# Kernel tuning notes

Measured on AMD Instinct MI355X. Metric: run time of the kernel, lower is better.

## Reference

```python
import jax, jax.numpy as jnp
from jax import lax
import numpy as np

NUM_ITER = 20
H, W = 512, 512
EPS = 1e-8

# fixed (non-trainable) kernels from the module
_GX = (1.0 / 6.0) * jnp.array([[-1.0, 0.0, 1.0], [-2.0, 0.0, 2.0], [-1.0, 0.0, 1.0]], jnp.float32)
_GY = (1.0 / 6.0) * jnp.array([[-1.0, -2.0, -1.0], [0.0, 0.0, 0.0], [1.0, 2.0, 1.0]], jnp.float32)
_GXU = jnp.array([[0.0, 0.0, 0.0], [0.0, -1.0, 1.0], [0.0, 0.0, 0.0]], jnp.float32)
_GYU = jnp.array([[0.0, 0.0, 0.0], [0.0, -1.0, 0.0], [0.0, 1.0, 0.0]], jnp.float32)
K_GRAD = jnp.stack([_GX, _GY])[:, None]    # (2,1,3,3) image-gradient conv
K_GRADU = jnp.stack([_GXU, _GYU])[:, None]  # (2,1,3,3) flow-gradient conv
K_AVG = jnp.ones((1, 1, 3, 3), jnp.float32) / 9.0  # AvgPool2d(3,1,1), count_include_pad
P33 = ((1, 1), (1, 1))
P13 = ((0, 0), (1, 1))
P31 = ((1, 1), (0, 0))


def _conv(x, w, pad):
    return lax.conv_general_dilated(x, w, (1, 1), padding=pad,
                                    dimension_numbers=('NCHW', 'OIHW', 'NCHW'))


def setup_inputs() -> dict:
    key = jax.random.key(0)
    x = jax.random.uniform(key, (4, 2, H, W), dtype=jnp.float32)  # two frames per sample
    return {
        'x': x,
        'lam': jnp.array([0.15], jnp.float32),
        'tau': jnp.array([0.25], jnp.float32),
        'theta': jnp.array([0.3], jnp.float32),
        'wx': jnp.array([[-1.0, 1.0, 0.0]], jnp.float32),   # trainable div_x kernel
        'wy': jnp.array([[-1.0], [1.0], [0.0]], jnp.float32),  # trainable div_y kernel
    }


def reference(x, lam, tau, theta, wx, wy):
    B = x.shape[0]
    Wx = wx.reshape(1, 1, 1, 3)
    Wy = wy.reshape(1, 1, 3, 1)
    rho_c = x[:, 1:2] - x[:, 0:1]                          # [B,1,H,W]
    grad_im = _conv(x[:, 1:2], K_GRAD, P33)                # [B,2,H,W]
    norm_grad = jnp.sum(grad_im * grad_im, axis=1, keepdims=True) + EPS  # [B,1,H,W]
    z = jnp.zeros_like(grad_im)

    def step(carry, _):
        u, p1, p2 = carry
        rho = rho_c + jnp.sum(grad_im * u, axis=1, keepdims=True)
        th = theta * lam * norm_grad
        v = u - jnp.where(jnp.abs(rho) < th,
                          rho * grad_im / norm_grad,
                          theta * lam * grad_im * jnp.sign(rho))
        div1 = _conv(p1[:, 0:1], Wx, P13) + _conv(p1[:, 1:2], Wy, P31)
        div2 = _conv(p2[:, 0:1], Wx, P13) + _conv(p2[:, 1:2], Wy, P31)
        u = jnp.concatenate([v[:, 0:1] + theta * div1,
                             v[:, 1:2] + theta * div2], axis=1)
        gu1 = _conv(u[:, 0:1], K_GRADU, P33)               # [B,2,H,W]
        gu2 = _conv(u[:, 1:2], K_GRADU, P33)
        r = tau / theta
        p1 = (p1 + r * gu1) / (1.0 + r * jnp.sum(jnp.abs(gu1), axis=1, keepdims=True))
        p2 = (p2 + r * gu2) / (1.0 + r * jnp.sum(jnp.abs(gu2), axis=1, keepdims=True))
        return (u, p1, p2), None

    (u, _, _), _ = lax.scan(step, (z, z, z), None, length=NUM_ITER)
    # AvgPool2d(3, stride=1, padding=1), applied depthwise
    out = _conv(u.reshape(B * 2, 1, H, W), K_AVG, P33).reshape(B, 2, H, W)
    return out
```

## Files before the change

kernel.cpp:

```cpp
#include <hip/hip_runtime.h>


#define HH 512
#define WW 512
#define BB 4
constexpr int HW   = HH * WW;
constexpr int NTOT = BB * HW;
constexpr float EPS = 1e-8f;

#define T 32
#define HALO_L 6
#define REG 48
#define NPX (REG * REG)
#define TPB 768
#define SLOTS 3
#define NBLK 1024
#define XR 50
#define XN (XR * XR)
#define XSL 4

__global__ __launch_bounds__(TPB, 1) void k_fused(
    const float* __restrict__ x,
    float2* __restrict__ ug, float4* __restrict__ pg,
    const float* __restrict__ lam_p, const float* __restrict__ tau_p,
    const float* __restrict__ theta_p,
    const float* __restrict__ wxp, const float* __restrict__ wyp,
    float* __restrict__ out, int phase)
{
    __shared__ float2 su[NPX];
    __shared__ float2 spa[NPX];
    __shared__ float2 spb[NPX];

    const int tid  = threadIdx.x;
    const int blk  = blockIdx.x;
    const int bimg = blk >> 8;
    const int t    = blk & 255;
    const int gi0  = (t >> 4) * T;
    const int gj0  = (t & 15) * T;

    const float lam = lam_p[0], theta = theta_p[0];
    const float r   = tau_p[0] / theta;
    const float tl  = theta * lam;
    const float wx0 = wxp[0], wx1 = wxp[1], wx2 = wxp[2];
    const float wy0 = wyp[0], wy1 = wyp[1], wy2 = wyp[2];

    const int gbase = bimg * HW;
    const float* x0p = x + (size_t)bimg * 2 * HW;
    const float* x1p = x0p + HW;

    int  lis[SLOTS], ljs[SLOTS], gofs[SLOTS];
    bool inb[SLOTS];
    float2 ruv[SLOTS], rpa[SLOTS], rpb[SLOTS];
    float  x0v[SLOTS];

    #pragma unroll
    for (int s = 0; s < SLOTS; ++s) {
        int idx = tid + s * TPB;
        int li = idx / REG, lj = idx - li * REG;
        lis[s] = li; ljs[s] = lj;
        int gi = gi0 + li - HALO_L, gj = gj0 + lj - HALO_L;
        bool in = ((unsigned)gi < HH) & ((unsigned)gj < WW);
        inb[s] = in;
        int gl = gi * WW + gj;
        gofs[s] = gl;
        float2 uv = make_float2(0.f, 0.f);
        float4 p4 = make_float4(0.f, 0.f, 0.f, 0.f);
        float xv = 0.f;
        if (in) {
            xv = x0p[gl];
            if (phase != 0) {
                uv = ug[gbase + gl];
                p4 = pg[gbase + gl];
            }
        }
        x0v[s] = xv;
        ruv[s] = uv;
        rpa[s] = make_float2(p4.x, p4.y);
        rpb[s] = make_float2(p4.z, p4.w);
    }
    #pragma unroll
    for (int s = 0; s < XSL; ++s) {
        int idx = tid + s * TPB;
        if (idx < XN) {
            int li = idx / XR, lj = idx - li * XR;
            int gi = gi0 + li - (HALO_L + 1), gj = gj0 + lj - (HALO_L + 1);
            bool in = ((unsigned)gi < HH) & ((unsigned)gj < WW);
            ((float*)spa)[idx] = in ? x1p[gi * WW + gj] : 0.f;
        }
    }
    __syncthreads();

    float rgx[SLOTS], rgy[SLOTS], rrc[SLOTS], rth[SLOTS], rnv[SLOTS];
    const float* stg = (const float*)spa;
    #pragma unroll
    for (int s = 0; s < SLOTS; ++s) {
        int sc = (lis[s] + 1) * XR + (ljs[s] + 1);
        float a00 = stg[sc - XR - 1], a01 = stg[sc - XR], a02 = stg[sc - XR + 1];
        float a10 = stg[sc - 1],      a11 = stg[sc],      a12 = stg[sc + 1];
        float a20 = stg[sc + XR - 1], a21 = stg[sc + XR], a22 = stg[sc + XR + 1];
        const float c6 = 1.f / 6.f;
        float gxv = c6 * (-a00 + a02 - 2.f * a10 + 2.f * a12 - a20 + a22);
        float gyv = c6 * (-a00 - 2.f * a01 - a02 + a20 + 2.f * a21 + a22);
        float nm  = gxv * gxv + gyv * gyv + EPS;
        rgx[s] = gxv; rgy[s] = gyv;
        rrc[s] = a11 - x0v[s];
        rth[s] = tl * nm;
        rnv[s] = __builtin_amdgcn_rcpf(nm);
    }
    __syncthreads();

    #pragma unroll
    for (int s = 0; s < SLOTS; ++s) {
        int idx = tid + s * TPB;
        su[idx]  = ruv[s];
        spa[idx] = rpa[s];
        spb[idx] = rpb[s];
    }
    __syncthreads();

    for (int k = 1; k <= 5; ++k) {
        const int lo = k, hi_u = REG - 2 * k;
        #pragma unroll
        for (int s = 0; s < SLOTS; ++s) {
            int idx = tid + s * TPB;
            int li = lis[s], lj = ljs[s];
            if (li < lo || li > hi_u || lj < lo || lj > hi_u) continue;
            float2 uv = ruv[s];
            float rho = rrc[s] + rgx[s] * uv.x + rgy[s] * uv.y;
            float d = (fabsf(rho) < rth[s]) ? rho * rnv[s] : copysignf(tl, rho);
            float v1 = uv.x - d * rgx[s];
            float v2 = uv.y - d * rgy[s];
            float2 pal = spa[idx - 1],   par = spa[idx + 1];
            float2 pbt = spb[idx - REG], pbb = spb[idx + REG];
            float2 pac = rpa[s],         pbc = rpb[s];
            float div1 = wx0 * pal.x + wx1 * pac.x + wx2 * par.x
                       + wy0 * pbt.x + wy1 * pbc.x + wy2 * pbb.x;
            float div2 = wx0 * pal.y + wx1 * pac.y + wx2 * par.y
                       + wy0 * pbt.y + wy1 * pbc.y + wy2 * pbb.y;
            float nu1 = v1 + theta * div1;
            float nu2 = v2 + theta * div2;
            if (!inb[s]) { nu1 = 0.f; nu2 = 0.f; }
            float2 nuv = make_float2(nu1, nu2);
            ruv[s] = nuv; su[idx] = nuv;
        }
        __syncthreads();
        if (phase == 2 && k == 5) break;

        const int hi_p = REG - 1 - 2 * k;
        #pragma unroll
        for (int s = 0; s < SLOTS; ++s) {
            int idx = tid + s * TPB;
            int li = lis[s], lj = ljs[s];
            if (li < lo || li > hi_p || lj < lo || lj > hi_p) continue;
            float2 uc = ruv[s];
            float2 uR = su[idx + 1];
            float2 uB = su[idx + REG];
            float gu1x = uR.x - uc.x, gu1y = uB.x - uc.x;
            float gu2x = uR.y - uc.y, gu2y = uB.y - uc.y;
            float d1 = 1.f + r * (fabsf(gu1x) + fabsf(gu1y));
            float id1 = __builtin_amdgcn_rcpf(d1);
            float np11 = (rpa[s].x + r * gu1x) * id1;
            float np12 = (rpb[s].x + r * gu1y) * id1;
            float d2 = 1.f + r * (fabsf(gu2x) + fabsf(gu2y));
            float id2 = __builtin_amdgcn_rcpf(d2);
            float np21 = (rpa[s].y + r * gu2x) * id2;
            float np22 = (rpb[s].y + r * gu2y) * id2;
            if (!inb[s]) { np11 = 0.f; np12 = 0.f; np21 = 0.f; np22 = 0.f; }
            float2 npa = make_float2(np11, np21);
            float2 npb = make_float2(np12, np22);
            rpa[s] = npa; rpb[s] = npb;
            spa[idx] = npa; spb[idx] = npb;
        }
        __syncthreads();
    }

    if (phase != 2) {
        #pragma unroll
        for (int s = 0; s < SLOTS; ++s) {
            int li = lis[s], lj = ljs[s];
            if (li < HALO_L || li >= HALO_L + T || lj < HALO_L || lj >= HALO_L + T) continue;
            int gl = gofs[s];
            ug[gbase + gl] = ruv[s];
            pg[gbase + gl] = make_float4(rpa[s].x, rpa[s].y, rpb[s].x, rpb[s].y);
        }
    } else {
        const float inv9 = 1.f / 9.f;
        #pragma unroll
        for (int s = 0; s < SLOTS; ++s) {
            int idx = tid + s * TPB;
            int li = lis[s], lj = ljs[s];
            if (li < HALO_L || li >= HALO_L + T || lj < HALO_L || lj >= HALO_L + T) continue;
            float2 a0 = su[idx - REG - 1], a1 = su[idx - REG], a2 = su[idx - REG + 1];
            float2 b0 = su[idx - 1],       b1 = su[idx],       b2 = su[idx + 1];
            float2 c0 = su[idx + REG - 1], c1 = su[idx + REG], c2 = su[idx + REG + 1];
            float s1 = a0.x + a1.x + a2.x + b0.x + b1.x + b2.x + c0.x + c1.x + c2.x;
            float s2 = a0.y + a1.y + a2.y + b0.y + b1.y + b2.y + c0.y + c1.y + c2.y;
            int gl = gofs[s];
            out[(size_t)bimg * 2 * HW + gl]      = s1 * inv9;
            out[(size_t)bimg * 2 * HW + HW + gl] = s2 * inv9;
        }
    }
}

extern "C" void kernel_launch(void* const* d_in, const int* in_sizes, int n_in,
                              void* d_out, int out_size, void* d_ws, size_t ws_size,
                              hipStream_t stream) {
    const float* x     = (const float*)d_in[0];
    const float* lam   = (const float*)d_in[1];
    const float* tau   = (const float*)d_in[2];
    const float* theta = (const float*)d_in[3];
    const float* wx    = (const float*)d_in[4];
    const float* wy    = (const float*)d_in[5];
    float* out = (float*)d_out;

    float*  ws = (float*)d_ws;
    float2* ug = (float2*)ws;
    float4* pg = (float4*)(ws + (size_t)2 * NTOT);

    for (int c = 0; c < 4; ++c) {
        int phase = (c == 0) ? 0 : (c == 3) ? 2 : 1;
        k_fused<<<dim3(NBLK), dim3(TPB), 0, stream>>>(
            x, ug, pg, lam, tau, theta, wx, wy, out, phase);
    }
}
```

Measured before the change: 177.4 us.

## Assign 2x2 pixel quads per thread with vectorized shared/global accesses

Each thread now owns a 2x2 block of pixels instead of three strided pixels, so horizontal and vertical neighbours inside the quad come from registers rather than LDS. Shared and global loads and stores become float4/float2 vectors, and the shrink-threshold branch is replaced by a clamp. The block drops to 576 threads with padded LDS arrays and a launch bound that permits more resident blocks. In exchange, register pressure per thread rises, and the coarser 2-pixel granularity does some redundant work at the shrinking valid-region edges.

```diff
diff --git a/kernel.cpp b/kernel.cpp
--- a/kernel.cpp
+++ b/kernel.cpp
@@ -12,14 +12,19 @@
 #define HALO_L 6
 #define REG 48
 #define NPX (REG * REG)
-#define TPB 768
-#define SLOTS 3
+#define TPB 576
+#define CW 24
 #define NBLK 1024
 #define XR 50
 #define XN (XR * XR)
-#define XSL 4
-
-__global__ __launch_bounds__(TPB, 1) void k_fused(
+#define XSL 5
+#define OFS (REG + 2)
+
+__device__ __forceinline__ float2 f2add(float2 a, float2 b) {
+    return make_float2(a.x + b.x, a.y + b.y);
+}
+
+__global__ __launch_bounds__(TPB, 5) void k_fused(
     const float* __restrict__ x,
     float2* __restrict__ ug, float4* __restrict__ pg,
     const float* __restrict__ lam_p, const float* __restrict__ tau_p,
@@ -27,9 +32,12 @@
     const float* __restrict__ wxp, const float* __restrict__ wyp,
     float* __restrict__ out, int phase)
 {
-    __shared__ float2 su[NPX];
-    __shared__ float2 spa[NPX];
-    __shared__ float2 spb[NPX];
+    __shared__ __align__(16) float2 su_s [NPX + 2 * OFS];
+    __shared__ __align__(16) float2 spa_s[NPX + 2 * OFS];
+    __shared__ __align__(16) float2 spb_s[NPX + 2 * OFS];
+    float2* su  = su_s  + OFS;
+    float2* spa = spa_s + OFS;
+    float2* spb = spb_s + OFS;
 
     const int tid  = threadIdx.x;
     const int blk  = blockIdx.x;
@@ -48,156 +56,236 @@
     const float* x0p = x + (size_t)bimg * 2 * HW;
     const float* x1p = x0p + HW;
 
-    int  lis[SLOTS], ljs[SLOTS], gofs[SLOTS];
-    bool inb[SLOTS];
-    float2 ruv[SLOTS], rpa[SLOTS], rpb[SLOTS];
-    float  x0v[SLOTS];
+    const int ci = tid / CW, cj = tid - ci * CW;
+    const int li = 2 * ci, lj = 2 * cj;
+    const int idx = li * REG + lj;
+    const int gi = gi0 + li - HALO_L, gj = gj0 + lj - HALO_L;
+    const int gl = gi * WW + gj;
+    const bool rin0 = ((unsigned)gi < HH);
+    const bool rin1 = ((unsigned)(gi + 1) < HH);
+    const bool cin  = ((unsigned)gj < WW);
+
+    float2 ruv[2][2], rpa[2][2], rpb[2][2];
+    float  x0v[2][2];
 
     #pragma unroll
-    for (int s = 0; s < SLOTS; ++s) {
-        int idx = tid + s * TPB;
-        int li = idx / REG, lj = idx - li * REG;
-        lis[s] = li; ljs[s] = lj;
-        int gi = gi0 + li - HALO_L, gj = gj0 + lj - HALO_L;
-        bool in = ((unsigned)gi < HH) & ((unsigned)gj < WW);
-        inb[s] = in;
-        int gl = gi * WW + gj;
-        gofs[s] = gl;
-        float2 uv = make_float2(0.f, 0.f);
-        float4 p4 = make_float4(0.f, 0.f, 0.f, 0.f);
-        float xv = 0.f;
-        if (in) {
-            xv = x0p[gl];
+    for (int rr = 0; rr < 2; ++rr) {
+        const bool rin = (rr == 0) ? rin0 : rin1;
+        float2 xp = make_float2(0.f, 0.f);
+        float4 uu = make_float4(0.f, 0.f, 0.f, 0.f);
+        float4 pa0 = make_float4(0.f, 0.f, 0.f, 0.f);
+        float4 pa1 = make_float4(0.f, 0.f, 0.f, 0.f);
+        if (rin & cin) {
+            const int go = gl + rr * WW;
+            xp = *(const float2*)(x0p + go);
             if (phase != 0) {
-                uv = ug[gbase + gl];
-                p4 = pg[gbase + gl];
-            }
-        }
-        x0v[s] = xv;
-        ruv[s] = uv;
-        rpa[s] = make_float2(p4.x, p4.y);
-        rpb[s] = make_float2(p4.z, p4.w);
+                uu  = *(const float4*)((const float*)(ug + gbase + go));
+                pa0 = pg[gbase + go];
+                pa1 = pg[gbase + go + 1];
+            }
+        }
+        x0v[rr][0] = xp.x;  x0v[rr][1] = xp.y;
+        ruv[rr][0] = make_float2(uu.x, uu.y);
+        ruv[rr][1] = make_float2(uu.z, uu.w);
+        rpa[rr][0] = make_float2(pa0.x, pa0.y);
+        rpb[rr][0] = make_float2(pa0.z, pa0.w);
+        rpa[rr][1] = make_float2(pa1.x, pa1.y);
+        rpb[rr][1] = make_float2(pa1.z, pa1.w);
     }
     #pragma unroll
     for (int s = 0; s < XSL; ++s) {
-        int idx = tid + s * TPB;
-        if (idx < XN) {
-            int li = idx / XR, lj = idx - li * XR;
-            int gi = gi0 + li - (HALO_L + 1), gj = gj0 + lj - (HALO_L + 1);
-            bool in = ((unsigned)gi < HH) & ((unsigned)gj < WW);
-            ((float*)spa)[idx] = in ? x1p[gi * WW + gj] : 0.f;
+        int idx2 = tid + s * TPB;
+        if (idx2 < XN) {
+            int li2 = idx2 / XR, lj2 = idx2 - li2 * XR;
+            int gi2 = gi0 + li2 - (HALO_L + 1), gj2 = gj0 + lj2 - (HALO_L + 1);
+            bool in = ((unsigned)gi2 < HH) & ((unsigned)gj2 < WW);
+            ((float*)spa_s)[idx2] = in ? x1p[gi2 * WW + gj2] : 0.f;
         }
     }
     __syncthreads();
 
-    float rgx[SLOTS], rgy[SLOTS], rrc[SLOTS], rth[SLOTS], rnv[SLOTS];
-    const float* stg = (const float*)spa;
+    float rgx[2][2], rgy[2][2], rrc[2][2], rnv[2][2];
+    {
+        const float* stg = (const float*)spa_s;
+        float w[4][4];
+        #pragma unroll
+        for (int ri = 0; ri < 4; ++ri) {
+            float2 p01 = *(const float2*)&stg[(li + ri) * XR + lj];
+            float2 p23 = *(const float2*)&stg[(li + ri) * XR + lj + 2];
+            w[ri][0] = p01.x; w[ri][1] = p01.y;
+            w[ri][2] = p23.x; w[ri][3] = p23.y;
+        }
+        const float c6 = 1.f / 6.f;
+        #pragma unroll
+        for (int rr = 0; rr < 2; ++rr) {
+            #pragma unroll
+            for (int cc = 0; cc < 2; ++cc) {
+                float a00 = w[rr][cc],     a01 = w[rr][cc + 1],     a02 = w[rr][cc + 2];
+                float a10 = w[rr + 1][cc], a11 = w[rr + 1][cc + 1], a12 = w[rr + 1][cc + 2];
+                float a20 = w[rr + 2][cc], a21 = w[rr + 2][cc + 1], a22 = w[rr + 2][cc + 2];
+                float gxv = c6 * (-a00 + a02 - 2.f * a10 + 2.f * a12 - a20 + a22);
+                float gyv = c6 * (-a00 - 2.f * a01 - a02 + a20 + 2.f * a21 + a22);
+                float nm  = gxv * gxv + gyv * gyv + EPS;
+                rgx[rr][cc] = gxv; rgy[rr][cc] = gyv;
+                rrc[rr][cc] = a11 - x0v[rr][cc];
+                rnv[rr][cc] = __builtin_amdgcn_rcpf(nm);
+            }
+        }
+    }
+    __syncthreads();
+
     #pragma unroll
-    for (int s = 0; s < SLOTS; ++s) {
-        int sc = (lis[s] + 1) * XR + (ljs[s] + 1);
-        float a00 = stg[sc - XR - 1], a01 = stg[sc - XR], a02 = stg[sc - XR + 1];
-        float a10 = stg[sc - 1],      a11 = stg[sc],      a12 = stg[sc + 1];
-        float a20 = stg[sc + XR - 1], a21 = stg[sc + XR], a22 = stg[sc + XR + 1];
-        const float c6 = 1.f / 6.f;
-        float gxv = c6 * (-a00 + a02 - 2.f * a10 + 2.f * a12 - a20 + a22);
-        float gyv = c6 * (-a00 - 2.f * a01 - a02 + a20 + 2.f * a21 + a22);
-        float nm  = gxv * gxv + gyv * gyv + EPS;
-        rgx[s] = gxv; rgy[s] = gyv;
-        rrc[s] = a11 - x0v[s];
-        rth[s] = tl * nm;
-        rnv[s] = __builtin_amdgcn_rcpf(nm);
-    }
-    __syncthreads();
-
-    #pragma unroll
-    for (int s = 0; s < SLOTS; ++s) {
-        int idx = tid + s * TPB;
-        su[idx]  = ruv[s];
-        spa[idx] = rpa[s];
-        spb[idx] = rpb[s];
+    for (int rr = 0; rr < 2; ++rr) {
+        const int ix = idx + rr * REG;
+        *(float4*)&su[ix]  = make_float4(ruv[rr][0].x, ruv[rr][0].y, ruv[rr][1].x, ruv[rr][1].y);
+        *(float4*)&spa[ix] = make_float4(rpa[rr][0].x, rpa[rr][0].y, rpa[rr][1].x, rpa[rr][1].y);
+        *(float4*)&spb[ix] = make_float4(rpb[rr][0].x, rpb[rr][0].y, rpb[rr][1].x, rpb[rr][1].y);
     }
     __syncthreads();
 
     for (int k = 1; k <= 5; ++k) {
         const int lo = k, hi_u = REG - 2 * k;
-        #pragma unroll
-        for (int s = 0; s < SLOTS; ++s) {
-            int idx = tid + s * TPB;
-            int li = lis[s], lj = ljs[s];
-            if (li < lo || li > hi_u || lj < lo || lj > hi_u) continue;
-            float2 uv = ruv[s];
-            float rho = rrc[s] + rgx[s] * uv.x + rgy[s] * uv.y;
-            float d = (fabsf(rho) < rth[s]) ? rho * rnv[s] : copysignf(tl, rho);
-            float v1 = uv.x - d * rgx[s];
-            float v2 = uv.y - d * rgy[s];
-            float2 pal = spa[idx - 1],   par = spa[idx + 1];
-            float2 pbt = spb[idx - REG], pbb = spb[idx + REG];
-            float2 pac = rpa[s],         pbc = rpb[s];
-            float div1 = wx0 * pal.x + wx1 * pac.x + wx2 * par.x
-                       + wy0 * pbt.x + wy1 * pbc.x + wy2 * pbb.x;
-            float div2 = wx0 * pal.y + wx1 * pac.y + wx2 * par.y
-                       + wy0 * pbt.y + wy1 * pbc.y + wy2 * pbb.y;
-            float nu1 = v1 + theta * div1;
-            float nu2 = v2 + theta * div2;
-            if (!inb[s]) { nu1 = 0.f; nu2 = 0.f; }
-            float2 nuv = make_float2(nu1, nu2);
-            ruv[s] = nuv; su[idx] = nuv;
+        if (li + 1 >= lo && li <= hi_u && lj + 1 >= lo && lj <= hi_u) {
+            bool vr[2], vc[2];
+            vr[0] = (li >= lo) && (li <= hi_u);
+            vr[1] = (li + 1 >= lo) && (li + 1 <= hi_u);
+            vc[0] = (lj >= lo) && (lj <= hi_u);
+            vc[1] = (lj + 1 >= lo) && (lj + 1 <= hi_u);
+            float2 paL0 = spa[idx - 1],       paL1 = spa[idx + REG - 1];
+            float2 paR0 = spa[idx + 2],       paR1 = spa[idx + REG + 2];
+            float4 pbT  = *(float4*)&spb[idx - REG];
+            float4 pbB  = *(float4*)&spb[idx + 2 * REG];
+            float2 nuv[2][2];
+            #pragma unroll
+            for (int rr = 0; rr < 2; ++rr) {
+                #pragma unroll
+                for (int cc = 0; cc < 2; ++cc) {
+                    float2 uv = ruv[rr][cc];
+                    float rho = rrc[rr][cc] + rgx[rr][cc] * uv.x + rgy[rr][cc] * uv.y;
+                    float tt = rho * rnv[rr][cc];
+                    float d  = fminf(fmaxf(tt, -tl), tl);
+                    float v1 = uv.x - d * rgx[rr][cc];
+                    float v2 = uv.y - d * rgy[rr][cc];
+                    float2 paLv = (cc == 0) ? ((rr == 0) ? paL0 : paL1) : rpa[rr][0];
+                    float2 paRv = (cc == 0) ? rpa[rr][1] : ((rr == 0) ? paR0 : paR1);
+                    float2 pbTv = (rr == 0) ? ((cc == 0) ? make_float2(pbT.x, pbT.y)
+                                                         : make_float2(pbT.z, pbT.w))
+                                            : rpb[0][cc];
+                    float2 pbBv = (rr == 0) ? rpb[1][cc]
+                                            : ((cc == 0) ? make_float2(pbB.x, pbB.y)
+                                                         : make_float2(pbB.z, pbB.w));
+                    float2 pac = rpa[rr][cc], pbc = rpb[rr][cc];
+                    float div1 = wx0 * paLv.x + wx1 * pac.x + wx2 * paRv.x
+                               + wy0 * pbTv.x + wy1 * pbc.x + wy2 * pbBv.x;
+                    float div2 = wx0 * paLv.y + wx1 * pac.y + wx2 * paRv.y
+                               + wy0 * pbTv.y + wy1 * pbc.y + wy2 * pbBv.y;
+                    float nu1 = v1 + theta * div1;
+                    float nu2 = v2 + theta * div2;
+                    const bool live = ((rr == 0) ? rin0 : rin1) && cin;
+                    if (!live) { nu1 = 0.f; nu2 = 0.f; }
+                    const bool valid = vr[rr] && vc[cc];
+                    nuv[rr][cc] = valid ? make_float2(nu1, nu2) : uv;
+                }
+            }
+            ruv[0][0] = nuv[0][0]; ruv[0][1] = nuv[0][1];
+            ruv[1][0] = nuv[1][0]; ruv[1][1] = nuv[1][1];
+            *(float4*)&su[idx]       = make_float4(nuv[0][0].x, nuv[0][0].y, nuv[0][1].x, nuv[0][1].y);
+            *(float4*)&su[idx + REG] = make_float4(nuv[1][0].x, nuv[1][0].y, nuv[1][1].x, nuv[1][1].y);
         }
         __syncthreads();
         if (phase == 2 && k == 5) break;
 
         const int hi_p = REG - 1 - 2 * k;
-        #pragma unroll
-        for (int s = 0; s < SLOTS; ++s) {
-            int idx = tid + s * TPB;
-            int li = lis[s], lj = ljs[s];
-            if (li < lo || li > hi_p || lj < lo || lj > hi_p) continue;
-            float2 uc = ruv[s];
-            float2 uR = su[idx + 1];
-            float2 uB = su[idx + REG];
-            float gu1x = uR.x - uc.x, gu1y = uB.x - uc.x;
-            float gu2x = uR.y - uc.y, gu2y = uB.y - uc.y;
-            float d1 = 1.f + r * (fabsf(gu1x) + fabsf(gu1y));
-            float id1 = __builtin_amdgcn_rcpf(d1);
-            float np11 = (rpa[s].x + r * gu1x) * id1;
-            float np12 = (rpb[s].x + r * gu1y) * id1;
-            float d2 = 1.f + r * (fabsf(gu2x) + fabsf(gu2y));
-            float id2 = __builtin_amdgcn_rcpf(d2);
-            float np21 = (rpa[s].y + r * gu2x) * id2;
-            float np22 = (rpb[s].y + r * gu2y) * id2;
-            if (!inb[s]) { np11 = 0.f; np12 = 0.f; np21 = 0.f; np22 = 0.f; }
-            float2 npa = make_float2(np11, np21);
-            float2 npb = make_float2(np12, np22);
-            rpa[s] = npa; rpb[s] = npb;
-            spa[idx] = npa; spb[idx] = npb;
+        if (li + 1 >= lo && li <= hi_p && lj + 1 >= lo && lj <= hi_p) {
+            bool vr[2], vc[2];
+            vr[0] = (li >= lo) && (li <= hi_p);
+            vr[1] = (li + 1 >= lo) && (li + 1 <= hi_p);
+            vc[0] = (lj >= lo) && (lj <= hi_p);
+            vc[1] = (lj + 1 >= lo) && (lj + 1 <= hi_p);
+            float2 uR0 = su[idx + 2], uR1 = su[idx + REG + 2];
+            float4 uB4 = *(float4*)&su[idx + 2 * REG];
+            float2 npa[2][2], npb[2][2];
+            #pragma unroll
+            for (int rr = 0; rr < 2; ++rr) {
+                #pragma unroll
+                for (int cc = 0; cc < 2; ++cc) {
+                    float2 uc  = ruv[rr][cc];
+                    float2 uRv = (cc == 0) ? ruv[rr][1] : ((rr == 0) ? uR0 : uR1);
+                    float2 uBv = (rr == 0) ? ruv[1][cc]
+                                           : ((cc == 0) ? make_float2(uB4.x, uB4.y)
+                                                        : make_float2(uB4.z, uB4.w));
+                    float gu1x = uRv.x - uc.x, gu1y = uBv.x - uc.x;
+                    float gu2x = uRv.y - uc.y, gu2y = uBv.y - uc.y;
+                    float d1 = 1.f + r * (fabsf(gu1x) + fabsf(gu1y));
+                    float id1 = __builtin_amdgcn_rcpf(d1);
+                    float np11 = (rpa[rr][cc].x + r * gu1x) * id1;
+                    float np12 = (rpb[rr][cc].x + r * gu1y) * id1;
+                    float d2 = 1.f + r * (fabsf(gu2x) + fabsf(gu2y));
+                    float id2 = __builtin_amdgcn_rcpf(d2);
+                    float np21 = (rpa[rr][cc].y + r * gu2x) * id2;
+                    float np22 = (rpb[rr][cc].y + r * gu2y) * id2;
+                    const bool live = ((rr == 0) ? rin0 : rin1) && cin;
+                    if (!live) { np11 = 0.f; np12 = 0.f; np21 = 0.f; np22 = 0.f; }
+                    const bool valid = vr[rr] && vc[cc];
+                    npa[rr][cc] = valid ? make_float2(np11, np21) : rpa[rr][cc];
+                    npb[rr][cc] = valid ? make_float2(np12, np22) : rpb[rr][cc];
+                }
+            }
+            rpa[0][0] = npa[0][0]; rpa[0][1] = npa[0][1];
+            rpa[1][0] = npa[1][0]; rpa[1][1] = npa[1][1];
+            rpb[0][0] = npb[0][0]; rpb[0][1] = npb[0][1];
+            rpb[1][0] = npb[1][0]; rpb[1][1] = npb[1][1];
+            *(float4*)&spa[idx]       = make_float4(npa[0][0].x, npa[0][0].y, npa[0][1].x, npa[0][1].y);
+            *(float4*)&spa[idx + REG] = make_float4(npa[1][0].x, npa[1][0].y, npa[1][1].x, npa[1][1].y);
+            *(float4*)&spb[idx]       = make_float4(npb[0][0].x, npb[0][0].y, npb[0][1].x, npb[0][1].y);
+            *(float4*)&spb[idx + REG] = make_float4(npb[1][0].x, npb[1][0].y, npb[1][1].x, npb[1][1].y);
         }
         __syncthreads();
     }
 
+    const bool interior = (li >= HALO_L) && (li <= HALO_L + T - 2)
+                        && (lj >= HALO_L) && (lj <= HALO_L + T - 2);
     if (phase != 2) {
-        #pragma unroll
-        for (int s = 0; s < SLOTS; ++s) {
-            int li = lis[s], lj = ljs[s];
-            if (li < HALO_L || li >= HALO_L + T || lj < HALO_L || lj >= HALO_L + T) continue;
-            int gl = gofs[s];
-            ug[gbase + gl] = ruv[s];
-            pg[gbase + gl] = make_float4(rpa[s].x, rpa[s].y, rpb[s].x, rpb[s].y);
+        if (interior) {
+            #pragma unroll
+            for (int rr = 0; rr < 2; ++rr) {
+                const int go = gl + rr * WW;
+                *(float4*)((float*)(ug + gbase + go)) =
+                    make_float4(ruv[rr][0].x, ruv[rr][0].y, ruv[rr][1].x, ruv[rr][1].y);
+                pg[gbase + go]     = make_float4(rpa[rr][0].x, rpa[rr][0].y, rpb[rr][0].x, rpb[rr][0].y);
+                pg[gbase + go + 1] = make_float4(rpa[rr][1].x, rpa[rr][1].y, rpb[rr][1].x, rpb[rr][1].y);
+            }
         }
     } else {
-        const float inv9 = 1.f / 9.f;
-        #pragma unroll
-        for (int s = 0; s < SLOTS; ++s) {
-            int idx = tid + s * TPB;
-            int li = lis[s], lj = ljs[s];
-            if (li < HALO_L || li >= HALO_L + T || lj < HALO_L || lj >= HALO_L + T) continue;
-            float2 a0 = su[idx - REG - 1], a1 = su[idx - REG], a2 = su[idx - REG + 1];
-            float2 b0 = su[idx - 1],       b1 = su[idx],       b2 = su[idx + 1];
-            float2 c0 = su[idx + REG - 1], c1 = su[idx + REG], c2 = su[idx + REG + 1];
-            float s1 = a0.x + a1.x + a2.x + b0.x + b1.x + b2.x + c0.x + c1.x + c2.x;
-            float s2 = a0.y + a1.y + a2.y + b0.y + b1.y + b2.y + c0.y + c1.y + c2.y;
-            int gl = gofs[s];
-            out[(size_t)bimg * 2 * HW + gl]      = s1 * inv9;
-            out[(size_t)bimg * 2 * HW + HW + gl] = s2 * inv9;
+        if (interior) {
+            const float inv9 = 1.f / 9.f;
+            float2 m[4][4];
+            #pragma unroll
+            for (int ri = 0; ri < 4; ++ri) {
+                const int bx = idx + (ri - 1) * REG;
+                float2 e0  = su[bx - 1];
+                float4 mid = *(float4*)&su[bx];
+                float2 e3  = su[bx + 2];
+                m[ri][0] = e0;
+                m[ri][1] = make_float2(mid.x, mid.y);
+                m[ri][2] = make_float2(mid.z, mid.w);
+                m[ri][3] = e3;
+            }
+            float2 tc[4][2];
+            #pragma unroll
+            for (int ri = 0; ri < 4; ++ri) {
+                tc[ri][0] = f2add(f2add(m[ri][0], m[ri][1]), m[ri][2]);
+                tc[ri][1] = f2add(f2add(m[ri][1], m[ri][2]), m[ri][3]);
+            }
+            const size_t obase = (size_t)bimg * 2 * HW;
+            #pragma unroll
+            for (int rr = 0; rr < 2; ++rr) {
+                float2 s0 = f2add(f2add(tc[rr][0], tc[rr + 1][0]), tc[rr + 2][0]);
+                float2 s1 = f2add(f2add(tc[rr][1], tc[rr + 1][1]), tc[rr + 2][1]);
+                const int go = gl + rr * WW;
+                *(float2*)(out + obase + go)      = make_float2(s0.x * inv9, s1.x * inv9);
+                *(float2*)(out + obase + HW + go) = make_float2(s0.y * inv9, s1.y * inv9);
+            }
         }
     }
 }
```

Measured after the change: 247.4 us. +39.4%, slower.
